# Kernel optimization log

Hardware: AMD Instinct MI355X
Metric: run time of the kernel (lower is better)

Reference implementation:

```python
import jax, jax.numpy as jnp
import numpy as np

SPARSITY = 0.1  # fraction k of weights kept (matches init sparsity)


def _subnet(scores, k):
    # Faithful to GetSubnet.forward: sort flattened scores ascending,
    # zero the bottom (1-k)*n entries, set the top k*n entries to 1.
    n = scores.size
    j = int((1.0 - k) * n)  # static under jit
    idx = jnp.argsort(scores.ravel())  # ascending, like torch .sort()
    flat = jnp.zeros((n,), scores.dtype).at[idx[j:]].set(1.0)
    return flat.reshape(scores.shape)


def setup_inputs() -> dict:
    key = jax.random.key(0)
    k1, k2 = jax.random.split(key)
    down_mask = jax.random.normal(k1, (8192, 2048), dtype=jnp.float32)
    up_mask = jax.random.normal(k2, (2048, 8192), dtype=jnp.float32)
    return {"down_mask": down_mask, "up_mask": up_mask}


def reference(down_mask, up_mask):
    # AdapterSubnet.forward: binary top-k masks of |down_mask| and |up_mask|
    return (_subnet(jnp.abs(down_mask), SPARSITY),
            _subnet(jnp.abs(up_mask), SPARSITY))
```

## Files before the change

kernel.cpp:

```cpp
#include <hip/hip_runtime.h>

using u32 = unsigned int;

#define H1_BINS 4096
#define H2_BINS 2048
#define H3_BINS 256
#define H1_OFF  0
#define H2_OFF  (H1_OFF + 2 * H1_BINS)
#define H3_OFF  (H2_OFF + 2 * H2_BINS)
#define SEL_OFF (H3_OFF + 2 * H3_BINS)
#define SEL_WORDS 8
#define CTR_OFF (SEL_OFF + 2 * SEL_WORDS)
#define CTR_WORDS 8
#define EQ_OFF  (CTR_OFF + CTR_WORDS)
#define EQ_CAP  4096
#define ZERO_WORDS EQ_OFF

#define CBUF 2048

__device__ __forceinline__ u32 absbits(u32 x) { return x & 0x7FFFFFFFu; }

template<int BINS>
__device__ void tail_select(u32* __restrict__ gh, u32 K, int pass,
                            u32* __restrict__ sel, u32* __restrict__ sh ) {
    constexpr int C = BINS / 256;
    const int tid = threadIdx.x;
    u32 Gprev = 0;
    if (pass == 1) Gprev = sel[2];
    else if (pass == 2) Gprev = sel[5];
    const u32 Krem = K - Gprev;

    u32 loc[C];
    u32 s = 0;
    const int base = tid * C;
#pragma unroll
    for (int i = 0; i < C; i++) { loc[i] = atomicAdd(&gh[base + i], 0u); s += loc[i]; }
    sh[tid] = s;
    __syncthreads();
    if (tid == 0) {
        u32 run = 0;
        for (int i = 255; i >= 0; i--) { u32 x = sh[i]; sh[i] = run; run += x; }
    }
    __syncthreads();
    u32 running = sh[tid];
#pragma unroll
    for (int b = C - 1; b >= 0; b--) {
        u32 c = loc[b];
        if (running < Krem && running + c >= Krem) {
            int bin = base + b;
            if (pass == 0)      { sel[0] = (u32)bin; sel[2] = running; }
            else if (pass == 1) { sel[1] = (u32)bin; sel[5] = Gprev + running; }
            else {
                sel[3] = (sel[0] << 19) | (sel[1] << 8) | (u32)bin;
                sel[4] = Krem - running;
            }
        }
        running += c;
    }
}

__global__ void k_hist1(const float* __restrict__ in0, const float* __restrict__ in1,
                        int n0, int n1, int K0, int K1, u32* __restrict__ ws) {
    __shared__ u32 h[H1_BINS];
    __shared__ u32 isLast;
    const int m = blockIdx.y;
    const u32* in = (const u32*)(m ? in1 : in0);
    const int n = m ? n1 : n0;
    const int n4 = n >> 2;
    for (int i = threadIdx.x; i < H1_BINS; i += blockDim.x) h[i] = 0;
    __syncthreads();
    const uint4* v = (const uint4*)in;
    const int stride = gridDim.x * blockDim.x;
    for (int i = blockIdx.x * blockDim.x + threadIdx.x; i < n4; i += stride) {
        uint4 x = v[i];
        atomicAdd(&h[absbits(x.x) >> 19], 1u);
        atomicAdd(&h[absbits(x.y) >> 19], 1u);
        atomicAdd(&h[absbits(x.z) >> 19], 1u);
        atomicAdd(&h[absbits(x.w) >> 19], 1u);
    }
    if (blockIdx.x == 0 && (int)threadIdx.x < (n & 3)) {
        u32 u = absbits(in[n4 * 4 + threadIdx.x]);
        atomicAdd(&h[u >> 19], 1u);
    }
    __syncthreads();
    u32* g = ws + H1_OFF + m * H1_BINS;
    for (int i = threadIdx.x; i < H1_BINS; i += blockDim.x)
        if (h[i]) atomicAdd(&g[i], h[i]);
    __syncthreads();
    if (threadIdx.x == 0) {
        __threadfence();
        u32 d = atomicAdd(&ws[CTR_OFF + 0 + m], 1u);
        isLast = (d == gridDim.x - 1) ? 1u : 0u;
    }
    __syncthreads();
    if (isLast) {
        u32* sel = ws + SEL_OFF + m * SEL_WORDS;
        tail_select<H1_BINS>(g, (u32)(m ? K1 : K0), 0, sel, h);
    }
}

__global__ void k_hist2(const float* __restrict__ in0, const float* __restrict__ in1,
                        u32* __restrict__ sc0, u32* __restrict__ sc1,
                        int n0, int n1, int K0, int K1, u32* __restrict__ ws) {
    __shared__ u32 h[H2_BINS];
    __shared__ u32 lbuf[CBUF];
    __shared__ u32 lcnt;
    __shared__ u32 gbase;
    __shared__ u32 isLast;
    const int m = blockIdx.y;
    const u32* in = (const u32*)(m ? in1 : in0);
    u32* scr = m ? sc1 : sc0;
    const int n = m ? n1 : n0;
    const int n4 = n >> 2;
    u32* sel = ws + SEL_OFF + m * SEL_WORDS;
    const u32 p1 = sel[0];
    for (int i = threadIdx.x; i < H2_BINS; i += blockDim.x) h[i] = 0;
    if (threadIdx.x == 0) lcnt = 0;
    __syncthreads();
    const uint4* v = (const uint4*)in;
    const int stride = gridDim.x * blockDim.x;
    const int i0 = blockIdx.x * blockDim.x + threadIdx.x;
    const int nIter = (n4 + stride - 1) / stride;
    for (int it = 0; it < nIter; ++it) {
        int i = i0 + it * stride;
        if (i < n4) {
            uint4 x = v[i];
            u32 a;
            a = absbits(x.x); if ((a >> 19) == p1) { atomicAdd(&h[(a >> 8) & 0x7FFu], 1u); u32 p = atomicAdd(&lcnt, 1u); lbuf[p] = a; }
            a = absbits(x.y); if ((a >> 19) == p1) { atomicAdd(&h[(a >> 8) & 0x7FFu], 1u); u32 p = atomicAdd(&lcnt, 1u); lbuf[p] = a; }
            a = absbits(x.z); if ((a >> 19) == p1) { atomicAdd(&h[(a >> 8) & 0x7FFu], 1u); u32 p = atomicAdd(&lcnt, 1u); lbuf[p] = a; }
            a = absbits(x.w); if ((a >> 19) == p1) { atomicAdd(&h[(a >> 8) & 0x7FFu], 1u); u32 p = atomicAdd(&lcnt, 1u); lbuf[p] = a; }
        }
        __syncthreads();
        if (lcnt >= CBUF - 1024) {
            u32 c = lcnt;
            if (threadIdx.x == 0) gbase = atomicAdd(&sel[7], c);
            __syncthreads();
            for (u32 j = threadIdx.x; j < c; j += blockDim.x) scr[gbase + j] = lbuf[j];
            __syncthreads();
            if (threadIdx.x == 0) lcnt = 0;
            __syncthreads();
        }
    }
    if (blockIdx.x == 0 && (int)threadIdx.x < (n & 3)) {
        u32 a = absbits(in[n4 * 4 + threadIdx.x]);
        if ((a >> 19) == p1) {
            atomicAdd(&h[(a >> 8) & 0x7FFu], 1u);
            u32 p = atomicAdd(&sel[7], 1u);
            scr[p] = a;
        }
    }
    __syncthreads();
    {
        u32 c = lcnt;
        if (c) {
            if (threadIdx.x == 0) gbase = atomicAdd(&sel[7], c);
            __syncthreads();
            for (u32 j = threadIdx.x; j < c; j += blockDim.x) scr[gbase + j] = lbuf[j];
        }
    }
    __syncthreads();
    u32* g = ws + H2_OFF + m * H2_BINS;
    for (int i = threadIdx.x; i < H2_BINS; i += blockDim.x)
        if (h[i]) atomicAdd(&g[i], h[i]);
    __syncthreads();
    if (threadIdx.x == 0) {
        __threadfence();
        u32 d = atomicAdd(&ws[CTR_OFF + 2 + m], 1u);
        isLast = (d == gridDim.x - 1) ? 1u : 0u;
    }
    __syncthreads();
    if (isLast) tail_select<H2_BINS>(g, (u32)(m ? K1 : K0), 1, sel, h);
}

__global__ void k_hist3(const u32* __restrict__ sc0, const u32* __restrict__ sc1,
                        int K0, int K1, u32* __restrict__ ws) {
    __shared__ u32 h[H3_BINS];
    __shared__ u32 sh[256];
    __shared__ u32 isLast;
    const int m = blockIdx.y;
    const u32* scr = m ? sc1 : sc0;
    u32* sel = ws + SEL_OFF + m * SEL_WORDS;
    const u32 E = sel[7];
    const u32 pre20 = (sel[0] << 11) | sel[1];
    for (int i = threadIdx.x; i < H3_BINS; i += blockDim.x) h[i] = 0;
    __syncthreads();
    const u32 stride = gridDim.x * blockDim.x;
    for (u32 i = blockIdx.x * blockDim.x + threadIdx.x; i < E; i += stride) {
        u32 a = scr[i];
        if ((a >> 8) == pre20) atomicAdd(&h[a & 0xFFu], 1u);
    }
    __syncthreads();
    u32* g = ws + H3_OFF + m * H3_BINS;
    for (int i = threadIdx.x; i < H3_BINS; i += blockDim.x)
        if (h[i]) atomicAdd(&g[i], h[i]);
    __syncthreads();
    if (threadIdx.x == 0) {
        __threadfence();
        u32 d = atomicAdd(&ws[CTR_OFF + 4 + m], 1u);
        isLast = (d == gridDim.x - 1) ? 1u : 0u;
    }
    __syncthreads();
    if (isLast) tail_select<H3_BINS>(g, (u32)(m ? K1 : K0), 2, sel, sh);
}

__global__ void k_mask(const float* __restrict__ in0, const float* __restrict__ in1,
                       float* __restrict__ out0, float* __restrict__ out1,
                       int n0, int n1, u32* __restrict__ ws) {
    const int m = blockIdx.y;
    const u32* in = (const u32*)(m ? in1 : in0);
    float* out = m ? out1 : out0;
    const int n = m ? n1 : n0;
    const int n4 = n >> 2;
    u32* sel = ws + SEL_OFF + m * SEL_WORDS;
    const u32 t = sel[3];
    u32* eq = ws + EQ_OFF + m * EQ_CAP;
    const uint4* v = (const uint4*)in;
    float4* o = (float4*)out;
    const int stride = gridDim.x * blockDim.x;
    for (int i = blockIdx.x * blockDim.x + threadIdx.x; i < n4; i += stride) {
        uint4 x = v[i];
        u32 a0 = absbits(x.x), a1 = absbits(x.y), a2 = absbits(x.z), a3 = absbits(x.w);
        float4 r;
        r.x = (a0 > t) ? 1.0f : 0.0f;
        r.y = (a1 > t) ? 1.0f : 0.0f;
        r.z = (a2 > t) ? 1.0f : 0.0f;
        r.w = (a3 > t) ? 1.0f : 0.0f;
        o[i] = r;
        if (a0 == t) { u32 p = atomicAdd(&sel[6], 1u); if (p < EQ_CAP) eq[p] = (u32)(4 * i + 0); }
        if (a1 == t) { u32 p = atomicAdd(&sel[6], 1u); if (p < EQ_CAP) eq[p] = (u32)(4 * i + 1); }
        if (a2 == t) { u32 p = atomicAdd(&sel[6], 1u); if (p < EQ_CAP) eq[p] = (u32)(4 * i + 2); }
        if (a3 == t) { u32 p = atomicAdd(&sel[6], 1u); if (p < EQ_CAP) eq[p] = (u32)(4 * i + 3); }
    }
    if (blockIdx.x == 0 && (int)threadIdx.x < (n & 3)) {
        int idx = n4 * 4 + threadIdx.x;
        u32 a = absbits(in[idx]);
        out[idx] = (a > t) ? 1.0f : 0.0f;
        if (a == t) { u32 p = atomicAdd(&sel[6], 1u); if (p < EQ_CAP) eq[p] = (u32)idx; }
    }
}

__global__ void k_tie(float* __restrict__ out0, float* __restrict__ out1, u32* __restrict__ ws) {
    const int m = blockIdx.x;
    float* out = m ? out1 : out0;
    u32* sel = ws + SEL_OFF + m * SEL_WORDS;
    u32 E = sel[6]; if (E > EQ_CAP) E = EQ_CAP;
    const u32 R = sel[4];
    const u32* eq = ws + EQ_OFF + m * EQ_CAP;
    for (u32 e = threadIdx.x; e < E; e += blockDim.x) {
        u32 idx = eq[e];
        u32 cnt = 0;
        for (u32 e2 = 0; e2 < E; e2++) cnt += (eq[e2] > idx) ? 1u : 0u;
        if (cnt < R) out[idx] = 1.0f;
    }
}

extern "C" void kernel_launch(void* const* d_in, const int* in_sizes, int n_in,
                              void* d_out, int out_size, void* d_ws, size_t ws_size,
                              hipStream_t stream) {
    const float* in0 = (const float*)d_in[0];
    const float* in1 = (const float*)d_in[1];
    const int n0 = in_sizes[0];
    const int n1 = in_sizes[1];
    float* out0 = (float*)d_out;
    float* out1 = out0 + n0;
    u32* ws = (u32*)d_ws;

    const double k = 0.1;
    const int j0 = (int)((1.0 - k) * (double)n0);
    const int j1 = (int)((1.0 - k) * (double)n1);
    const int K0 = n0 - j0;
    const int K1 = n1 - j1;

    u32* scr0 = (u32*)out0;
    u32* scr1 = (u32*)out1;

    hipMemsetAsync(ws, 0, ZERO_WORDS * sizeof(u32), stream);

    dim3 hgrid(1024, 2);
    k_hist1<<<hgrid, 256, 0, stream>>>(in0, in1, n0, n1, K0, K1, ws);
    k_hist2<<<hgrid, 256, 0, stream>>>(in0, in1, scr0, scr1, n0, n1, K0, K1, ws);
    k_hist3<<<dim3(32, 2), 256, 0, stream>>>(scr0, scr1, K0, K1, ws);
    k_mask<<<dim3(1024, 2), 256, 0, stream>>>(in0, in1, out0, out1, n0, n1, ws);
    k_tie<<<2, 256, 0, stream>>>(out0, out1, ws);
}
```

Before: 410.7 us.

## Replace radix passes two and three with compaction plus single-block two-level select

The second histogram pass now only compacts elements whose top bits match the pivot bin, with no shared-memory histogram atomics. A new single-block-per-matrix kernel does the remaining 19-bit select in two sub-passes (8192 then 64 bins) over the compacted buffer. That replaces the earlier hist2 tail select and the 32-block hist3. Histogram, compaction and mask loops are unrolled 8x/4x to keep more loads in flight, and mask outputs use nontemporal stores. The cost is a serial single-block select whose time grows with the compacted candidate count, plus a larger shared-memory staging buffer.

```diff
diff --git a/kernel.cpp b/kernel.cpp
--- a/kernel.cpp
+++ b/kernel.cpp
@@ -1,40 +1,30 @@
 #include <hip/hip_runtime.h>
 
 using u32 = unsigned int;
+typedef float f32x4 __attribute__((ext_vector_type(4)));
 
 #define H1_BINS 4096
-#define H2_BINS 2048
-#define H3_BINS 256
 #define H1_OFF  0
-#define H2_OFF  (H1_OFF + 2 * H1_BINS)
-#define H3_OFF  (H2_OFF + 2 * H2_BINS)
-#define SEL_OFF (H3_OFF + 2 * H3_BINS)
+#define SEL_OFF (H1_OFF + 2 * H1_BINS)
 #define SEL_WORDS 8
 #define CTR_OFF (SEL_OFF + 2 * SEL_WORDS)
-#define CTR_WORDS 8
-#define EQ_OFF  (CTR_OFF + CTR_WORDS)
+#define EQ_OFF  (CTR_OFF + 8)
 #define EQ_CAP  4096
 #define ZERO_WORDS EQ_OFF
 
-#define CBUF 2048
+#define CBUF    9216
+#define CTHRESH 1024
 
 __device__ __forceinline__ u32 absbits(u32 x) { return x & 0x7FFFFFFFu; }
 
-template<int BINS>
-__device__ void tail_select(u32* __restrict__ gh, u32 K, int pass,
-                            u32* __restrict__ sel, u32* __restrict__ sh ) {
-    constexpr int C = BINS / 256;
+__device__ void select_p1(u32* __restrict__ gh, u32 K, u32* __restrict__ sel,
+                          u32* __restrict__ sh ) {
     const int tid = threadIdx.x;
-    u32 Gprev = 0;
-    if (pass == 1) Gprev = sel[2];
-    else if (pass == 2) Gprev = sel[5];
-    const u32 Krem = K - Gprev;
-
-    u32 loc[C];
+    u32 loc[16];
     u32 s = 0;
-    const int base = tid * C;
-#pragma unroll
-    for (int i = 0; i < C; i++) { loc[i] = atomicAdd(&gh[base + i], 0u); s += loc[i]; }
+    const int base = tid * 16;
+#pragma unroll
+    for (int i = 0; i < 16; i++) { loc[i] = atomicAdd(&gh[base + i], 0u); s += loc[i]; }
     sh[tid] = s;
     __syncthreads();
     if (tid == 0) {
@@ -44,16 +34,11 @@
     __syncthreads();
     u32 running = sh[tid];
 #pragma unroll
-    for (int b = C - 1; b >= 0; b--) {
+    for (int b = 15; b >= 0; b--) {
         u32 c = loc[b];
-        if (running < Krem && running + c >= Krem) {
-            int bin = base + b;
-            if (pass == 0)      { sel[0] = (u32)bin; sel[2] = running; }
-            else if (pass == 1) { sel[1] = (u32)bin; sel[5] = Gprev + running; }
-            else {
-                sel[3] = (sel[0] << 19) | (sel[1] << 8) | (u32)bin;
-                sel[4] = Krem - running;
-            }
+        if (running < K && running + c >= K) {
+            sel[0] = (u32)(base + b);
+            sel[2] = running;
         }
         running += c;
     }
@@ -71,7 +56,20 @@
     __syncthreads();
     const uint4* v = (const uint4*)in;
     const int stride = gridDim.x * blockDim.x;
-    for (int i = blockIdx.x * blockDim.x + threadIdx.x; i < n4; i += stride) {
+    int i = blockIdx.x * blockDim.x + threadIdx.x;
+    for (; i + 7 * stride < n4; i += 8 * stride) {
+        uint4 x[8];
+#pragma unroll
+        for (int k = 0; k < 8; k++) x[k] = v[i + k * stride];
+#pragma unroll
+        for (int k = 0; k < 8; k++) {
+            atomicAdd(&h[absbits(x[k].x) >> 19], 1u);
+            atomicAdd(&h[absbits(x[k].y) >> 19], 1u);
+            atomicAdd(&h[absbits(x[k].z) >> 19], 1u);
+            atomicAdd(&h[absbits(x[k].w) >> 19], 1u);
+        }
+    }
+    for (; i < n4; i += stride) {
         uint4 x = v[i];
         atomicAdd(&h[absbits(x.x) >> 19], 1u);
         atomicAdd(&h[absbits(x.y) >> 19], 1u);
@@ -84,29 +82,23 @@
     }
     __syncthreads();
     u32* g = ws + H1_OFF + m * H1_BINS;
-    for (int i = threadIdx.x; i < H1_BINS; i += blockDim.x)
-        if (h[i]) atomicAdd(&g[i], h[i]);
+    for (int b = threadIdx.x; b < H1_BINS; b += blockDim.x)
+        if (h[b]) atomicAdd(&g[b], h[b]);
     __syncthreads();
     if (threadIdx.x == 0) {
         __threadfence();
-        u32 d = atomicAdd(&ws[CTR_OFF + 0 + m], 1u);
+        u32 d = atomicAdd(&ws[CTR_OFF + m], 1u);
         isLast = (d == gridDim.x - 1) ? 1u : 0u;
     }
     __syncthreads();
-    if (isLast) {
-        u32* sel = ws + SEL_OFF + m * SEL_WORDS;
-        tail_select<H1_BINS>(g, (u32)(m ? K1 : K0), 0, sel, h);
-    }
-}
-
-__global__ void k_hist2(const float* __restrict__ in0, const float* __restrict__ in1,
-                        u32* __restrict__ sc0, u32* __restrict__ sc1,
-                        int n0, int n1, int K0, int K1, u32* __restrict__ ws) {
-    __shared__ u32 h[H2_BINS];
+    if (isLast) select_p1(g, (u32)(m ? K1 : K0), ws + SEL_OFF + m * SEL_WORDS, h);
+}
+
+__global__ void k_compact(const float* __restrict__ in0, const float* __restrict__ in1,
+                          u32* __restrict__ sc0, u32* __restrict__ sc1,
+                          int n0, int n1, u32* __restrict__ ws) {
     __shared__ u32 lbuf[CBUF];
-    __shared__ u32 lcnt;
-    __shared__ u32 gbase;
-    __shared__ u32 isLast;
+    __shared__ u32 lcnt, gbase;
     const int m = blockIdx.y;
     const u32* in = (const u32*)(m ? in1 : in0);
     u32* scr = m ? sc1 : sc0;
@@ -114,94 +106,143 @@
     const int n4 = n >> 2;
     u32* sel = ws + SEL_OFF + m * SEL_WORDS;
     const u32 p1 = sel[0];
-    for (int i = threadIdx.x; i < H2_BINS; i += blockDim.x) h[i] = 0;
-    if (threadIdx.x == 0) lcnt = 0;
+    u32* cnt = &sel[7];
+    const int tid = threadIdx.x;
+    if (tid == 0) lcnt = 0;
     __syncthreads();
     const uint4* v = (const uint4*)in;
     const int stride = gridDim.x * blockDim.x;
-    const int i0 = blockIdx.x * blockDim.x + threadIdx.x;
-    const int nIter = (n4 + stride - 1) / stride;
+    const int i0 = blockIdx.x * blockDim.x + tid;
+    const int nIter = (n4 + 8 * stride - 1) / (8 * stride);
     for (int it = 0; it < nIter; ++it) {
-        int i = i0 + it * stride;
-        if (i < n4) {
-            uint4 x = v[i];
-            u32 a;
-            a = absbits(x.x); if ((a >> 19) == p1) { atomicAdd(&h[(a >> 8) & 0x7FFu], 1u); u32 p = atomicAdd(&lcnt, 1u); lbuf[p] = a; }
-            a = absbits(x.y); if ((a >> 19) == p1) { atomicAdd(&h[(a >> 8) & 0x7FFu], 1u); u32 p = atomicAdd(&lcnt, 1u); lbuf[p] = a; }
-            a = absbits(x.z); if ((a >> 19) == p1) { atomicAdd(&h[(a >> 8) & 0x7FFu], 1u); u32 p = atomicAdd(&lcnt, 1u); lbuf[p] = a; }
-            a = absbits(x.w); if ((a >> 19) == p1) { atomicAdd(&h[(a >> 8) & 0x7FFu], 1u); u32 p = atomicAdd(&lcnt, 1u); lbuf[p] = a; }
+        int i = i0 + it * 8 * stride;
+        if (i + 7 * stride < n4) {
+            uint4 x[8];
+#pragma unroll
+            for (int k = 0; k < 8; k++) x[k] = v[i + k * stride];
+#pragma unroll
+            for (int k = 0; k < 8; k++) {
+                u32 a;
+                a = absbits(x[k].x); if ((a >> 19) == p1) { u32 p = atomicAdd(&lcnt, 1u); lbuf[p] = a; }
+                a = absbits(x[k].y); if ((a >> 19) == p1) { u32 p = atomicAdd(&lcnt, 1u); lbuf[p] = a; }
+                a = absbits(x[k].z); if ((a >> 19) == p1) { u32 p = atomicAdd(&lcnt, 1u); lbuf[p] = a; }
+                a = absbits(x[k].w); if ((a >> 19) == p1) { u32 p = atomicAdd(&lcnt, 1u); lbuf[p] = a; }
+            }
+        } else {
+            for (int k = 0; k < 8; k++) {
+                int ii = i + k * stride;
+                if (ii < n4) {
+                    uint4 x = v[ii];
+                    u32 a;
+                    a = absbits(x.x); if ((a >> 19) == p1) { u32 p = atomicAdd(&lcnt, 1u); lbuf[p] = a; }
+                    a = absbits(x.y); if ((a >> 19) == p1) { u32 p = atomicAdd(&lcnt, 1u); lbuf[p] = a; }
+                    a = absbits(x.z); if ((a >> 19) == p1) { u32 p = atomicAdd(&lcnt, 1u); lbuf[p] = a; }
+                    a = absbits(x.w); if ((a >> 19) == p1) { u32 p = atomicAdd(&lcnt, 1u); lbuf[p] = a; }
+                }
+            }
         }
         __syncthreads();
-        if (lcnt >= CBUF - 1024) {
+        if (lcnt >= CTHRESH) {
             u32 c = lcnt;
-            if (threadIdx.x == 0) gbase = atomicAdd(&sel[7], c);
+            if (tid == 0) gbase = atomicAdd(cnt, c);
             __syncthreads();
-            for (u32 j = threadIdx.x; j < c; j += blockDim.x) scr[gbase + j] = lbuf[j];
+            for (u32 j = tid; j < c; j += blockDim.x) scr[gbase + j] = lbuf[j];
             __syncthreads();
-            if (threadIdx.x == 0) lcnt = 0;
-            __syncthreads();
-        }
-    }
-    if (blockIdx.x == 0 && (int)threadIdx.x < (n & 3)) {
-        u32 a = absbits(in[n4 * 4 + threadIdx.x]);
-        if ((a >> 19) == p1) {
-            atomicAdd(&h[(a >> 8) & 0x7FFu], 1u);
-            u32 p = atomicAdd(&sel[7], 1u);
-            scr[p] = a;
-        }
-    }
-    __syncthreads();
-    {
-        u32 c = lcnt;
-        if (c) {
-            if (threadIdx.x == 0) gbase = atomicAdd(&sel[7], c);
-            __syncthreads();
-            for (u32 j = threadIdx.x; j < c; j += blockDim.x) scr[gbase + j] = lbuf[j];
-        }
-    }
-    __syncthreads();
-    u32* g = ws + H2_OFF + m * H2_BINS;
-    for (int i = threadIdx.x; i < H2_BINS; i += blockDim.x)
-        if (h[i]) atomicAdd(&g[i], h[i]);
-    __syncthreads();
-    if (threadIdx.x == 0) {
-        __threadfence();
-        u32 d = atomicAdd(&ws[CTR_OFF + 2 + m], 1u);
-        isLast = (d == gridDim.x - 1) ? 1u : 0u;
-    }
-    __syncthreads();
-    if (isLast) tail_select<H2_BINS>(g, (u32)(m ? K1 : K0), 1, sel, h);
-}
-
-__global__ void k_hist3(const u32* __restrict__ sc0, const u32* __restrict__ sc1,
-                        int K0, int K1, u32* __restrict__ ws) {
-    __shared__ u32 h[H3_BINS];
-    __shared__ u32 sh[256];
-    __shared__ u32 isLast;
-    const int m = blockIdx.y;
+            if (tid == 0) lcnt = 0;
+        }
+        __syncthreads();
+    }
+    if (blockIdx.x == 0 && tid < (n & 3)) {
+        u32 a = absbits(in[n4 * 4 + tid]);
+        if ((a >> 19) == p1) { u32 p = atomicAdd(cnt, 1u); scr[p] = a; }
+    }
+    __syncthreads();
+    u32 c = lcnt;
+    if (c) {
+        if (tid == 0) gbase = atomicAdd(cnt, c);
+        __syncthreads();
+        for (u32 j = tid; j < c; j += blockDim.x) scr[gbase + j] = lbuf[j];
+    }
+}
+
+__global__ void k_select2(const u32* __restrict__ sc0, const u32* __restrict__ sc1,
+                          int K0, int K1, u32* __restrict__ ws) {
+    __shared__ u32 h[8192];
+    __shared__ u32 sh[1024];
+    __shared__ u32 g32[32];
+    __shared__ u32 selb1, selk2;
+    const int m = blockIdx.x;
     const u32* scr = m ? sc1 : sc0;
     u32* sel = ws + SEL_OFF + m * SEL_WORDS;
     const u32 E = sel[7];
-    const u32 pre20 = (sel[0] << 11) | sel[1];
-    for (int i = threadIdx.x; i < H3_BINS; i += blockDim.x) h[i] = 0;
-    __syncthreads();
-    const u32 stride = gridDim.x * blockDim.x;
-    for (u32 i = blockIdx.x * blockDim.x + threadIdx.x; i < E; i += stride) {
-        u32 a = scr[i];
-        if ((a >> 8) == pre20) atomicAdd(&h[a & 0xFFu], 1u);
-    }
-    __syncthreads();
-    u32* g = ws + H3_OFF + m * H3_BINS;
-    for (int i = threadIdx.x; i < H3_BINS; i += blockDim.x)
-        if (h[i]) atomicAdd(&g[i], h[i]);
-    __syncthreads();
-    if (threadIdx.x == 0) {
-        __threadfence();
-        u32 d = atomicAdd(&ws[CTR_OFF + 4 + m], 1u);
-        isLast = (d == gridDim.x - 1) ? 1u : 0u;
-    }
-    __syncthreads();
-    if (isLast) tail_select<H3_BINS>(g, (u32)(m ? K1 : K0), 2, sel, sh);
+    const u32 Krem = (u32)(m ? K1 : K0) - sel[2];
+    const int tid = threadIdx.x;
+    for (int i = tid; i < 8192; i += 1024) h[i] = 0;
+    __syncthreads();
+    u32 e = (u32)tid;
+    for (; e + 7u * 1024u < E; e += 8u * 1024u) {
+        u32 a[8];
+#pragma unroll
+        for (int k = 0; k < 8; k++) a[k] = scr[e + (u32)k * 1024u];
+#pragma unroll
+        for (int k = 0; k < 8; k++) atomicAdd(&h[(a[k] & 0x7FFFFu) >> 6], 1u);
+    }
+    for (; e < E; e += 1024u) atomicAdd(&h[(scr[e] & 0x7FFFFu) >> 6], 1u);
+    __syncthreads();
+    u32 loc[8];
+    u32 s = 0;
+    const int base = tid * 8;
+#pragma unroll
+    for (int i = 0; i < 8; i++) { loc[i] = h[base + i]; s += loc[i]; }
+    sh[tid] = s;
+    __syncthreads();
+    if (tid < 32) { u32 t = 0; for (int j = 0; j < 32; j++) t += sh[tid * 32 + j]; g32[tid] = t; }
+    __syncthreads();
+    if (tid == 0) { u32 run = 0; for (int j = 31; j >= 0; j--) { u32 x = g32[j]; g32[j] = run; run += x; } }
+    __syncthreads();
+    u32 running = g32[tid >> 5];
+    for (int j = (tid | 31); j > tid; j--) running += sh[j];
+#pragma unroll
+    for (int b = 7; b >= 0; b--) {
+        u32 c = loc[b];
+        if (running < Krem && running + c >= Krem) {
+            selb1 = (u32)(base + b);
+            selk2 = Krem - running;
+        }
+        running += c;
+    }
+    __syncthreads();
+    const u32 b1 = selb1;
+    const u32 K2 = selk2;
+    if (tid < 64) h[tid] = 0;
+    __syncthreads();
+    e = (u32)tid;
+    for (; e + 7u * 1024u < E; e += 8u * 1024u) {
+        u32 a[8];
+#pragma unroll
+        for (int k = 0; k < 8; k++) a[k] = scr[e + (u32)k * 1024u];
+#pragma unroll
+        for (int k = 0; k < 8; k++) {
+            u32 sfx = a[k] & 0x7FFFFu;
+            if ((sfx >> 6) == b1) atomicAdd(&h[sfx & 63u], 1u);
+        }
+    }
+    for (; e < E; e += 1024u) {
+        u32 sfx = scr[e] & 0x7FFFFu;
+        if ((sfx >> 6) == b1) atomicAdd(&h[sfx & 63u], 1u);
+    }
+    __syncthreads();
+    if (tid == 0) {
+        u32 run = 0, t6 = 0, R = 0;
+        for (int b = 63; b >= 0; b--) {
+            u32 c = h[b];
+            if (run < K2 && run + c >= K2) { t6 = (u32)b; R = K2 - run; }
+            run += c;
+        }
+        u32 t19 = (b1 << 6) | t6;
+        sel[3] = (sel[0] << 19) | t19;
+        sel[4] = R;
+    }
 }
 
 __global__ void k_mask(const float* __restrict__ in0, const float* __restrict__ in1,
@@ -216,17 +257,38 @@
     const u32 t = sel[3];
     u32* eq = ws + EQ_OFF + m * EQ_CAP;
     const uint4* v = (const uint4*)in;
-    float4* o = (float4*)out;
+    f32x4* o = (f32x4*)out;
     const int stride = gridDim.x * blockDim.x;
-    for (int i = blockIdx.x * blockDim.x + threadIdx.x; i < n4; i += stride) {
+    int i = blockIdx.x * blockDim.x + threadIdx.x;
+    for (; i + 3 * stride < n4; i += 4 * stride) {
+        uint4 x[4];
+#pragma unroll
+        for (int k = 0; k < 4; k++) x[k] = v[i + k * stride];
+#pragma unroll
+        for (int k = 0; k < 4; k++) {
+            u32 a0 = absbits(x[k].x), a1 = absbits(x[k].y), a2 = absbits(x[k].z), a3 = absbits(x[k].w);
+            f32x4 r;
+            r.x = (a0 > t) ? 1.0f : 0.0f;
+            r.y = (a1 > t) ? 1.0f : 0.0f;
+            r.z = (a2 > t) ? 1.0f : 0.0f;
+            r.w = (a3 > t) ? 1.0f : 0.0f;
+            __builtin_nontemporal_store(r, &o[i + k * stride]);
+            int ib = 4 * (i + k * stride);
+            if (a0 == t) { u32 p = atomicAdd(&sel[6], 1u); if (p < EQ_CAP) eq[p] = (u32)(ib + 0); }
+            if (a1 == t) { u32 p = atomicAdd(&sel[6], 1u); if (p < EQ_CAP) eq[p] = (u32)(ib + 1); }
+            if (a2 == t) { u32 p = atomicAdd(&sel[6], 1u); if (p < EQ_CAP) eq[p] = (u32)(ib + 2); }
+            if (a3 == t) { u32 p = atomicAdd(&sel[6], 1u); if (p < EQ_CAP) eq[p] = (u32)(ib + 3); }
+        }
+    }
+    for (; i < n4; i += stride) {
         uint4 x = v[i];
         u32 a0 = absbits(x.x), a1 = absbits(x.y), a2 = absbits(x.z), a3 = absbits(x.w);
-        float4 r;
+        f32x4 r;
         r.x = (a0 > t) ? 1.0f : 0.0f;
         r.y = (a1 > t) ? 1.0f : 0.0f;
         r.z = (a2 > t) ? 1.0f : 0.0f;
         r.w = (a3 > t) ? 1.0f : 0.0f;
-        o[i] = r;
+        __builtin_nontemporal_store(r, &o[i]);
         if (a0 == t) { u32 p = atomicAdd(&sel[6], 1u); if (p < EQ_CAP) eq[p] = (u32)(4 * i + 0); }
         if (a1 == t) { u32 p = atomicAdd(&sel[6], 1u); if (p < EQ_CAP) eq[p] = (u32)(4 * i + 1); }
         if (a2 == t) { u32 p = atomicAdd(&sel[6], 1u); if (p < EQ_CAP) eq[p] = (u32)(4 * i + 2); }
@@ -275,12 +337,11 @@
     u32* scr0 = (u32*)out0;
     u32* scr1 = (u32*)out1;
 
-    hipMemsetAsync(ws, 0, ZERO_WORDS * sizeof(u32), stream);
-
-    dim3 hgrid(1024, 2);
-    k_hist1<<<hgrid, 256, 0, stream>>>(in0, in1, n0, n1, K0, K1, ws);
-    k_hist2<<<hgrid, 256, 0, stream>>>(in0, in1, scr0, scr1, n0, n1, K0, K1, ws);
-    k_hist3<<<dim3(32, 2), 256, 0, stream>>>(scr0, scr1, K0, K1, ws);
-    k_mask<<<dim3(1024, 2), 256, 0, stream>>>(in0, in1, out0, out1, n0, n1, ws);
-    k_tie<<<2, 256, 0, stream>>>(out0, out1, ws);
-}
+    (void)hipMemsetAsync(ws, 0, ZERO_WORDS * sizeof(u32), stream);
+
+    k_hist1 <<<dim3(1024, 2), 256, 0, stream>>>(in0, in1, n0, n1, K0, K1, ws);
+    k_compact<<<dim3(1024, 2), 256, 0, stream>>>(in0, in1, scr0, scr1, n0, n1, ws);
+    k_select2<<<2, 1024, 0, stream>>>(scr0, scr1, K0, K1, ws);
+    k_mask   <<<dim3(1024, 2), 256, 0, stream>>>(in0, in1, out0, out1, n0, n1, ws);
+    k_tie    <<<2, 256, 0, stream>>>(out0, out1, ws);
+}
```

After: 387.8 us. 1.06x faster.
